# Performance work log

Measured on AMD Instinct MI355X. Metric: run time of the kernel, lower is better.

## Reference

```python
import jax, jax.numpy as jnp
import numpy as np

N_NODES = 100000

def setup_inputs() -> dict:
    key = jax.random.key(0)
    ks = jax.random.split(key, 8)
    n_feat, nhid, nclass = 256, 128, 40
    n_edges = 1600000
    x = jax.random.normal(ks[0], (N_NODES, n_feat), dtype=jnp.float32)
    edge_index = jax.random.randint(ks[1], (2, n_edges), 0, N_NODES, dtype=jnp.int64)
    # Glorot-ish scaled weights
    W1 = jax.random.normal(ks[2], (n_feat, nhid), dtype=jnp.float32) / np.sqrt(n_feat)
    b1 = jnp.zeros((nhid,), dtype=jnp.float32)
    W2 = jax.random.normal(ks[3], (nhid, nhid), dtype=jnp.float32) / np.sqrt(nhid)
    b2 = jnp.zeros((nhid,), dtype=jnp.float32)
    Wc = jax.random.normal(ks[4], (nhid, nclass), dtype=jnp.float32) / np.sqrt(nhid)
    bc = jnp.zeros((nclass,), dtype=jnp.float32)
    return {"x": x, "edge_index": edge_index, "W1": W1, "b1": b1,
            "W2": W2, "b2": b2, "Wc": Wc, "bc": bc}


def _gcn_conv(x, src, dst, W, b, n_nodes):
    """PyG GCNConv: transform, then sym-normalized aggregation with self-loops.
    out_i = sum_{j in N(i) u {i}} (d_i^-1/2 d_j^-1/2) (x_j W) + b,
    where d = in-degree over A + I.
    """
    h = x @ W  # [N, out]
    ones = jnp.ones_like(dst, dtype=h.dtype)
    deg = jax.ops.segment_sum(ones, dst, num_segments=n_nodes) + 1.0  # + self loop
    dinv = jax.lax.rsqrt(deg)  # deg >= 1, always valid
    norm = dinv[src] * dinv[dst]  # [E]
    msg = h[src] * norm[:, None]  # [E, out]  (dominant gather traffic)
    agg = jax.ops.segment_sum(msg, dst, num_segments=n_nodes)
    agg = agg + h * (dinv * dinv)[:, None]  # self-loop contribution
    return agg + b


def reference(x, edge_index, W1, b1, W2, b2, Wc, bc):
    # eval mode: dropout is identity
    src, dst = edge_index[0], edge_index[1]
    n = x.shape[0]
    h = jax.nn.relu(_gcn_conv(x, src, dst, W1, b1, n))
    h = jax.nn.relu(_gcn_conv(h, src, dst, W2, b2, n))
    return h @ Wc + bc
```

## Files before the change

### kernel.cpp

```cpp
#include <hip/hip_runtime.h>
#include <hip/hip_bf16.h>
#include <hip/hip_fp16.h>
#include <type_traits>


typedef _Float16 half8 __attribute__((ext_vector_type(8)));
typedef _Float16 half4v __attribute__((ext_vector_type(4)));
typedef float floatx4 __attribute__((ext_vector_type(4)));

#define EPB 8192


__device__ inline int block_incl_scan_256(int t, int* tmp) {
    int tid = threadIdx.x;
    tmp[tid] = t;
    __syncthreads();
    #pragma unroll
    for (int off = 1; off < 256; off <<= 1) {
        int v = (tid >= off) ? tmp[tid - off] : 0;
        __syncthreads();
        tmp[tid] += v;
        __syncthreads();
    }
    return tmp[tid];
}

template <int ITEMS>
__global__ __launch_bounds__(256) void k_scan1(const int* __restrict__ v,
                                               int* __restrict__ bsum, int n) {
    __shared__ int tmp[256];
    int base = blockIdx.x * (256 * ITEMS) + threadIdx.x * ITEMS;
    int t = 0;
    #pragma unroll
    for (int l = 0; l < ITEMS; ++l) {
        int i = base + l;
        t += (i < n) ? v[i] : 0;
    }
    block_incl_scan_256(t, tmp);
    if (threadIdx.x == 0) bsum[blockIdx.x] = tmp[255];
}

__global__ __launch_bounds__(256) void k_scan2(int* __restrict__ bsum, int nb) {
    __shared__ int tmp[256];
    int tid = threadIdx.x;
    int v = (tid < nb) ? bsum[tid] : 0;
    block_incl_scan_256(v, tmp);
    if (tid < nb) bsum[tid] = tid ? tmp[tid - 1] : 0;
}

template <int ITEMS>
__global__ __launch_bounds__(256) void k_scan3(const int* __restrict__ vin,
                                               const int* __restrict__ bsum,
                                               int* __restrict__ rp, int n) {
    __shared__ int tmp[256];
    int base = blockIdx.x * (256 * ITEMS) + threadIdx.x * ITEMS;
    int v[ITEMS];
    int t = 0;
    #pragma unroll
    for (int l = 0; l < ITEMS; ++l) {
        int i = base + l;
        v[l] = (i < n) ? vin[i] : 0;
        t += v[l];
    }
    block_incl_scan_256(t, tmp);
    int run = bsum[blockIdx.x] + (threadIdx.x ? tmp[threadIdx.x - 1] : 0);
    #pragma unroll
    for (int l = 0; l < ITEMS; ++l) {
        int i = base + l;
        if (i < n) rp[i] = run;
        run += v[l];
    }
}


__global__ __launch_bounds__(256) void k_histA(const int* __restrict__ dst,
                                               int* __restrict__ histM,
                                               int E, int nblk) {
    __shared__ int h[512];
    int tid = threadIdx.x;
    for (int i = tid; i < 512; i += 256) h[i] = 0;
    __syncthreads();
    int base = blockIdx.x * EPB;
    #pragma unroll 4
    for (int l = 0; l < EPB / 256; ++l) {
        int i = base + l * 256 + tid;
        if (i < E) atomicAdd(&h[dst[i] >> 8], 1);
    }
    __syncthreads();
    for (int i = tid; i < 512; i += 256)
        histM[i * nblk + blockIdx.x] = h[i];
}

__global__ __launch_bounds__(256) void k_scatterA(const int* __restrict__ src,
                                                  const int* __restrict__ dst,
                                                  const int* __restrict__ histS,
                                                  unsigned long long* __restrict__ eB,
                                                  int E, int nblk) {
    __shared__ int bse[512];
    __shared__ int cnt[512];
    int tid = threadIdx.x;
    for (int i = tid; i < 512; i += 256) {
        bse[i] = histS[i * nblk + blockIdx.x];
        cnt[i] = 0;
    }
    __syncthreads();
    int base = blockIdx.x * EPB;
    #pragma unroll 4
    for (int l = 0; l < EPB / 256; ++l) {
        int i = base + l * 256 + tid;
        if (i < E) {
            int d = dst[i];
            int s = src[i];
            int b = d >> 8;
            int r = atomicAdd(&cnt[b], 1);
            eB[bse[b] + r] = ((unsigned long long)(unsigned)d << 32) | (unsigned)s;
        }
    }
}

#define BCAP 4608
__global__ __launch_bounds__(256) void k_sortB(const unsigned long long* __restrict__ eB,
                                               const int* __restrict__ histS,
                                               int* __restrict__ srcS,
                                               int* __restrict__ rowptr,
                                               float* __restrict__ dinv,
                                               int n, int E, int nblk) {
    const int b   = blockIdx.x;
    const int tid = threadIdx.x;
    const int ni0 = b << 8;
    int s0 = histS[b * nblk];
    int s1 = (b < 511) ? histS[(b + 1) * nblk] : E;
    int cnt = s1 - s0;
    if (cnt > BCAP) cnt = BCAP;
    if (cnt == 0 && ni0 > n) return;

    __shared__ int hist[256];
    __shared__ int tmp[256];
    __shared__ int baseA[256];
    __shared__ int cntA[256];
    __shared__ int dstL[BCAP];
    __shared__ unsigned srcL[BCAP];
    __shared__ int lbA[256];

    hist[tid] = 0;
    cntA[tid] = 0;
    __syncthreads();
    for (int i = s0 + tid; i < s0 + cnt; i += 256) {
        int d = (int)(eB[i] >> 32);
        atomicAdd(&hist[d & 255], 1);
    }
    __syncthreads();
    int own  = hist[tid];
    int incl = block_incl_scan_256(own, tmp);
    baseA[tid] = incl - own;
    __syncthreads();
    for (int i = s0 + tid; i < s0 + cnt; i += 256) {
        unsigned long long v = eB[i];
        int d = (int)(v >> 32);
        int dig = d & 255;
        int r = atomicAdd(&cntA[dig], 1);
        int pos = baseA[dig] + r;
        dstL[pos] = d;
        srcL[pos] = (unsigned)v;
    }
    __syncthreads();
    for (int j = tid; j < cnt; j += 256)
        srcS[s0 + j] = (int)srcL[j];
    if (ni0 <= n) {
        int i = ni0 + tid;
        int lo = 0, hi = cnt;
        while (lo < hi) {
            int mid = (lo + hi) >> 1;
            if (dstL[mid] < i) lo = mid + 1; else hi = mid;
        }
        lbA[tid] = lo;
        __syncthreads();
        if (i <= n) {
            rowptr[i] = s0 + lo;
            if (i < n) {
                int ub = (tid < 255) ? lbA[tid + 1] : cnt;
                dinv[i] = rsqrtf((float)(ub - lo + 1));
            }
        }
    }
}

__global__ __launch_bounds__(256) void k_wcast(const float* __restrict__ W,
                                               _Float16* __restrict__ Wt,
                                               int N, int K, int kbits, int total) {
    int i = blockIdx.x * 256 + threadIdx.x;
    if (i < total) {
        int c = i >> kbits;
        int k = i & (K - 1);
        Wt[i] = (c < N) ? (_Float16)W[(size_t)k * N + c] : (_Float16)0.f;
    }
}


template <int K, int BN, typename AT, typename OT>
__global__ __launch_bounds__(256) void gemm_mfma(const AT* __restrict__ A,
                                                 const _Float16* __restrict__ Wt,
                                                 const float* __restrict__ bias,
                                                 OT* __restrict__ C,
                                                 int M, int N) {
    constexpr int NT = BN / 16;
    __shared__ __align__(16) _Float16 As[64][40];
    __shared__ __align__(16) _Float16 Bs[BN][40];

    const int tid  = threadIdx.x;
    const int bm   = blockIdx.x * 64;
    const int lane = tid & 63;
    const int wv   = tid >> 6;
    const int qd   = lane >> 4;
    const int ln15 = lane & 15;

    floatx4 acc[NT];
    #pragma unroll
    for (int c = 0; c < NT; ++c) acc[c] = (floatx4){0.f, 0.f, 0.f, 0.f};

    for (int k0 = 0; k0 < K; k0 += 32) {
        if constexpr (std::is_same<AT, float>::value) {
            #pragma unroll
            for (int l = 0; l < 2; ++l) {
                int f4  = tid + l * 256;
                int row = f4 >> 3;
                int kk  = (f4 & 7) << 2;
                float4 v = make_float4(0.f, 0.f, 0.f, 0.f);
                if (bm + row < M)
                    v = *(const float4*)(A + (size_t)(bm + row) * K + k0 + kk);
                half4v h;
                h[0] = (_Float16)v.x; h[1] = (_Float16)v.y;
                h[2] = (_Float16)v.z; h[3] = (_Float16)v.w;
                *(half4v*)&As[row][kk] = h;
            }
        } else {
            int row = tid >> 2;
            int kk  = (tid & 3) << 3;
            uint4 v = make_uint4(0u, 0u, 0u, 0u);
            if (bm + row < M)
                v = *(const uint4*)((const _Float16*)A + (size_t)(bm + row) * K + k0 + kk);
            *(uint4*)&As[row][kk] = v;
        }
        #pragma unroll
        for (int l = 0; l < (BN * 4 + 255) / 256; ++l) {
            int idx = tid + l * 256;
            if (idx < BN * 4) {
                int col = idx >> 2;
                int kk  = (idx & 3) << 3;
                *(uint4*)&Bs[col][kk] =
                    *(const uint4*)(Wt + (size_t)col * K + k0 + kk);
            }
        }
        __syncthreads();

        half8 a = *(const half8*)&As[wv * 16 + ln15][qd * 8];
        #pragma unroll
        for (int c = 0; c < NT; ++c) {
            half8 b = *(const half8*)&Bs[c * 16 + ln15][qd * 8];
            acc[c] = __builtin_amdgcn_mfma_f32_16x16x32_f16(a, b, acc[c], 0, 0, 0);
        }
        __syncthreads();
    }

    int baseRow = bm + wv * 16 + qd * 4;
    #pragma unroll
    for (int c = 0; c < NT; ++c) {
        int col = c * 16 + ln15;
        if constexpr (std::is_same<OT, _Float16>::value) {
            #pragma unroll
            for (int r = 0; r < 4; ++r) {
                int row = baseRow + r;
                if (row < M) C[(size_t)row * N + col] = (_Float16)acc[c][r];
            }
        } else {
            float bv = (col < N && bias) ? bias[col] : 0.f;
            #pragma unroll
            for (int r = 0; r < 4; ++r) {
                int row = baseRow + r;
                if (row < M && col < N)
                    ((float*)C)[(size_t)row * N + col] = acc[c][r] + bv;
            }
        }
    }
}


__global__ __launch_bounds__(256) void gcn_agg(const unsigned int* __restrict__ h,
                                               const int* __restrict__ rowptr,
                                               const int* __restrict__ srcS,
                                               const float* __restrict__ dinv,
                                               const float* __restrict__ bias,
                                               unsigned int* __restrict__ out,
                                               int n, int do_relu) {
    int node = blockIdx.x * 4 + (threadIdx.x >> 6);
    if (node >= n) return;
    const int lane = threadIdx.x & 63;
    const int g    = lane >> 4;
    const int t    = lane & 15;

    const _Float16* hb = (const _Float16*)h;

    float di = dinv[node];
    int e0 = rowptr[node];
    int e1 = rowptr[node + 1];

    half8 sv = *(const half8*)(hb + (size_t)(unsigned)node * 128 + t * 8);
    const float4* b4 = (const float4*)bias;
    float4 blo = b4[t * 2 + 0];
    float4 bhi = b4[t * 2 + 1];

    float acc[8];
    #pragma unroll
    for (int i = 0; i < 8; ++i) acc[i] = 0.f;

    for (int ce = e0; ce < e1; ce += 64) {
        int cnt = e1 - ce;
        cnt = (cnt < 64) ? cnt : 64;
        int colv = 0, wval = 0;
        if (lane < cnt) {
            int c = srcS[ce + lane];
            colv = c;
            wval = __float_as_int(di * dinv[c]);
        }
        #pragma unroll 2
        for (int d = 0; d < cnt; d += 4) {
            int idx = (d + g) << 2;
            int c   = __builtin_amdgcn_ds_bpermute(idx, colv);
            float w = __int_as_float(__builtin_amdgcn_ds_bpermute(idx, wval));
            half8 hv = *(const half8*)(hb + (size_t)(unsigned)c * 128 + t * 8);
            #pragma unroll
            for (int i = 0; i < 8; ++i)
                acc[i] += (float)hv[i] * w;
        }
    }

    #pragma unroll
    for (int i = 0; i < 8; ++i) acc[i] += __shfl_xor(acc[i], 16);
    #pragma unroll
    for (int i = 0; i < 8; ++i) acc[i] += __shfl_xor(acc[i], 32);

    float s = di * di;
    float bb[8] = {blo.x, blo.y, blo.z, blo.w, bhi.x, bhi.y, bhi.z, bhi.w};
    half8 o;
    #pragma unroll
    for (int i = 0; i < 8; ++i) {
        float v = acc[i] + (float)sv[i] * s + bb[i];
        if (do_relu) v = fmaxf(v, 0.f);
        o[i] = (_Float16)v;
    }
    if (g == 0)
        *(half8*)((_Float16*)out + (size_t)(unsigned)node * 128 + t * 8) = o;
}


extern "C" void kernel_launch(void* const* d_in, const int* in_sizes, int n_in,
                              void* d_out, int out_size, void* d_ws, size_t ws_size,
                              hipStream_t stream) {
    const float* x  = (const float*)d_in[0];
    const int* eidx = (const int*)d_in[1];
    const float* W1 = (const float*)d_in[2];
    const float* b1 = (const float*)d_in[3];
    const float* W2 = (const float*)d_in[4];
    const float* b2 = (const float*)d_in[5];
    const float* Wc = (const float*)d_in[6];
    const float* bc = (const float*)d_in[7];
    float* out = (float*)d_out;

    const int NF = 256, NH = 128, NC = 40;
    const int n = in_sizes[0] / NF;
    const int E = in_sizes[1] / 2;
    const int* src = eidx;
    const int* dst = eidx + E;

    const int nblk = (E + EPB - 1) / EPB;
    const int hm   = 512 * nblk;
    const int nbA  = (hm + 4095) / 4096;

    char* wsb = (char*)d_ws;
    size_t off = 0;
    auto alloc = [&](size_t bytes) {
        char* p = wsb + off;
        off = (off + bytes + 511) & ~(size_t)511;
        return p;
    };
    _Float16* hbuf = (_Float16*)alloc((size_t)n * NH * 2);
    _Float16* abuf = (_Float16*)alloc((size_t)n * NH * 2);
    _Float16* W1t  = (_Float16*)alloc((size_t)128 * 256 * 2);
    _Float16* W2t  = (_Float16*)alloc((size_t)128 * 128 * 2);
    _Float16* Wct  = (_Float16*)alloc((size_t)48 * 128 * 2);
    unsigned long long* eB = (unsigned long long*)alloc((size_t)E * 8);
    int* srcS      = (int*)alloc((size_t)E * 4);
    int* histM     = (int*)alloc((size_t)hm * 4);
    int* histS     = (int*)alloc((size_t)hm * 4);
    int* rowptr    = (int*)alloc((size_t)(n + 1) * 4);
    float* dinv    = (float*)alloc((size_t)n * 4);
    int* bsumA     = (int*)alloc(1024);

    k_histA<<<nblk, 256, 0, stream>>>(dst, histM, E, nblk);
    k_scan1<16><<<nbA, 256, 0, stream>>>(histM, bsumA, hm);
    k_scan2<<<1, 256, 0, stream>>>(bsumA, nbA);
    k_scan3<16><<<nbA, 256, 0, stream>>>(histM, bsumA, histS, hm);
    k_scatterA<<<nblk, 256, 0, stream>>>(src, dst, histS, eB, E, nblk);
    k_sortB<<<512, 256, 0, stream>>>(eB, histS, srcS, rowptr, dinv, n, E, nblk);

    k_wcast<<<(128 * 256 + 255) / 256, 256, 0, stream>>>(W1, W1t, 128, 256, 8, 128 * 256);
    k_wcast<<<(128 * 128 + 255) / 256, 256, 0, stream>>>(W2, W2t, 128, 128, 7, 128 * 128);
    k_wcast<<<(48 * 128 + 255) / 256, 256, 0, stream>>>(Wc, Wct, 40, 128, 7, 48 * 128);

    const int gMt = (n + 63) / 64;
    gemm_mfma<256, 128, float, _Float16><<<gMt, 256, 0, stream>>>(x, W1t, nullptr, hbuf, n, NH);
    gcn_agg<<<(n + 3) / 4, 256, 0, stream>>>((const unsigned int*)hbuf, rowptr, srcS, dinv, b1,
                                             (unsigned int*)abuf, n, 1);
    gemm_mfma<128, 128, _Float16, _Float16><<<gMt, 256, 0, stream>>>(abuf, W2t, nullptr, hbuf, n, NH);
    gcn_agg<<<(n + 3) / 4, 256, 0, stream>>>((const unsigned int*)hbuf, rowptr, srcS, dinv, b2,
                                             (unsigned int*)abuf, n, 1);
    gemm_mfma<128, 48, _Float16, float><<<gMt, 256, 0, stream>>>(abuf, Wct, bc, out, n, NC);
}
```

Measured before the change: 418.1 us.

## Keep full weight matrix resident in LDS and load A fragments directly

```diff
diff --git a/kernel.cpp b/kernel.cpp
--- a/kernel.cpp
+++ b/kernel.cpp
@@ -197,88 +197,95 @@
 }
 
 
-template <int K, int BN, typename AT, typename OT>
-__global__ __launch_bounds__(256) void gemm_mfma(const AT* __restrict__ A,
+template <int K, int BN, int MT, typename AT, typename OT>
+__global__ __launch_bounds__(256) void gemm_bres(const AT* __restrict__ A,
                                                  const _Float16* __restrict__ Wt,
                                                  const float* __restrict__ bias,
                                                  OT* __restrict__ C,
                                                  int M, int N) {
+    constexpr int KP = K + 8;
     constexpr int NT = BN / 16;
-    __shared__ __align__(16) _Float16 As[64][40];
-    __shared__ __align__(16) _Float16 Bs[BN][40];
+    __shared__ __align__(16) _Float16 Bs[BN * KP];
 
     const int tid  = threadIdx.x;
-    const int bm   = blockIdx.x * 64;
     const int lane = tid & 63;
     const int wv   = tid >> 6;
     const int qd   = lane >> 4;
     const int ln15 = lane & 15;
-
-    floatx4 acc[NT];
-    #pragma unroll
-    for (int c = 0; c < NT; ++c) acc[c] = (floatx4){0.f, 0.f, 0.f, 0.f};
-
-    for (int k0 = 0; k0 < K; k0 += 32) {
-        if constexpr (std::is_same<AT, float>::value) {
-            #pragma unroll
-            for (int l = 0; l < 2; ++l) {
-                int f4  = tid + l * 256;
-                int row = f4 >> 3;
-                int kk  = (f4 & 7) << 2;
-                float4 v = make_float4(0.f, 0.f, 0.f, 0.f);
-                if (bm + row < M)
-                    v = *(const float4*)(A + (size_t)(bm + row) * K + k0 + kk);
-                half4v h;
-                h[0] = (_Float16)v.x; h[1] = (_Float16)v.y;
-                h[2] = (_Float16)v.z; h[3] = (_Float16)v.w;
-                *(half4v*)&As[row][kk] = h;
+    const int bm   = blockIdx.x * (64 * MT);
+
+    constexpr int TOT = BN * K / 8;
+    for (int i = tid; i < TOT; i += 256) {
+        int idx = i * 8;
+        int col = idx / K;
+        int kk  = idx % K;
+        *(uint4*)&Bs[col * KP + kk] = *(const uint4*)(Wt + idx);
+    }
+    __syncthreads();
+
+    floatx4 acc[MT][NT];
+    #pragma unroll
+    for (int mt = 0; mt < MT; ++mt)
+        #pragma unroll
+        for (int c = 0; c < NT; ++c) acc[mt][c] = (floatx4){0.f, 0.f, 0.f, 0.f};
+
+    int rw[MT];
+    #pragma unroll
+    for (int mt = 0; mt < MT; ++mt) {
+        int r = bm + (wv * MT + mt) * 16 + ln15;
+        rw[mt] = (r < M) ? r : (M - 1);
+    }
+
+    #pragma unroll
+    for (int ks = 0; ks < K / 32; ++ks) {
+        half8 a[MT];
+        #pragma unroll
+        for (int mt = 0; mt < MT; ++mt) {
+            if constexpr (std::is_same<AT, float>::value) {
+                const float* p = A + (size_t)rw[mt] * K + ks * 32 + qd * 8;
+                float4 v0 = *(const float4*)p;
+                float4 v1 = *(const float4*)(p + 4);
+                half8 h;
+                h[0] = (_Float16)v0.x; h[1] = (_Float16)v0.y;
+                h[2] = (_Float16)v0.z; h[3] = (_Float16)v0.w;
+                h[4] = (_Float16)v1.x; h[5] = (_Float16)v1.y;
+                h[6] = (_Float16)v1.z; h[7] = (_Float16)v1.w;
+                a[mt] = h;
+            } else {
+                a[mt] = *(const half8*)((const _Float16*)A +
+                                        (size_t)rw[mt] * K + ks * 32 + qd * 8);
             }
-        } else {
-            int row = tid >> 2;
-            int kk  = (tid & 3) << 3;
-            uint4 v = make_uint4(0u, 0u, 0u, 0u);
-            if (bm + row < M)
-                v = *(const uint4*)((const _Float16*)A + (size_t)(bm + row) * K + k0 + kk);
-            *(uint4*)&As[row][kk] = v;
-        }
-        #pragma unroll
-        for (int l = 0; l < (BN * 4 + 255) / 256; ++l) {
-            int idx = tid + l * 256;
-            if (idx < BN * 4) {
-                int col = idx >> 2;
-                int kk  = (idx & 3) << 3;
-                *(uint4*)&Bs[col][kk] =
-                    *(const uint4*)(Wt + (size_t)col * K + k0 + kk);
-            }
-        }
-        __syncthreads();
-
-        half8 a = *(const half8*)&As[wv * 16 + ln15][qd * 8];
+        }
         #pragma unroll
         for (int c = 0; c < NT; ++c) {
-            half8 b = *(const half8*)&Bs[c * 16 + ln15][qd * 8];
-            acc[c] = __builtin_amdgcn_mfma_f32_16x16x32_f16(a, b, acc[c], 0, 0, 0);
-        }
-        __syncthreads();
-    }
-
-    int baseRow = bm + wv * 16 + qd * 4;
-    #pragma unroll
-    for (int c = 0; c < NT; ++c) {
-        int col = c * 16 + ln15;
-        if constexpr (std::is_same<OT, _Float16>::value) {
-            #pragma unroll
-            for (int r = 0; r < 4; ++r) {
-                int row = baseRow + r;
-                if (row < M) C[(size_t)row * N + col] = (_Float16)acc[c][r];
-            }
-        } else {
-            float bv = (col < N && bias) ? bias[col] : 0.f;
-            #pragma unroll
-            for (int r = 0; r < 4; ++r) {
-                int row = baseRow + r;
-                if (row < M && col < N)
-                    ((float*)C)[(size_t)row * N + col] = acc[c][r] + bv;
+            half8 b = *(const half8*)&Bs[(c * 16 + ln15) * KP + ks * 32 + qd * 8];
+            #pragma unroll
+            for (int mt = 0; mt < MT; ++mt)
+                acc[mt][c] = __builtin_amdgcn_mfma_f32_16x16x32_f16(a[mt], b,
+                                                                    acc[mt][c], 0, 0, 0);
+        }
+    }
+
+    #pragma unroll
+    for (int mt = 0; mt < MT; ++mt) {
+        int baseRow = bm + (wv * MT + mt) * 16 + qd * 4;
+        #pragma unroll
+        for (int c = 0; c < NT; ++c) {
+            int col = c * 16 + ln15;
+            if constexpr (std::is_same<OT, _Float16>::value) {
+                #pragma unroll
+                for (int r = 0; r < 4; ++r) {
+                    int row = baseRow + r;
+                    if (row < M) C[(size_t)row * N + col] = (_Float16)acc[mt][c][r];
+                }
+            } else {
+                float bv = (col < N && bias) ? bias[col] : 0.f;
+                #pragma unroll
+                for (int r = 0; r < 4; ++r) {
+                    int row = baseRow + r;
+                    if (row < M && col < N)
+                        ((float*)C)[(size_t)row * N + col] = acc[mt][c][r] + bv;
+                }
             }
         }
     }
@@ -322,8 +329,38 @@
             colv = c;
             wval = __float_as_int(di * dinv[c]);
         }
-        #pragma unroll 2
-        for (int d = 0; d < cnt; d += 4) {
+        int d = 0;
+        for (; d + 16 <= cnt; d += 16) {
+            int i0 = (d + 0 + g) << 2;
+            int i1 = (d + 4 + g) << 2;
+            int i2 = (d + 8 + g) << 2;
+            int i3 = (d + 12 + g) << 2;
+            int c0 = __builtin_amdgcn_ds_bpermute(i0, colv);
+            int c1 = __builtin_amdgcn_ds_bpermute(i1, colv);
+            int c2 = __builtin_amdgcn_ds_bpermute(i2, colv);
+            int c3 = __builtin_amdgcn_ds_bpermute(i3, colv);
+            int w0i = __builtin_amdgcn_ds_bpermute(i0, wval);
+            int w1i = __builtin_amdgcn_ds_bpermute(i1, wval);
+            int w2i = __builtin_amdgcn_ds_bpermute(i2, wval);
+            int w3i = __builtin_amdgcn_ds_bpermute(i3, wval);
+            half8 h0 = *(const half8*)(hb + (size_t)(unsigned)c0 * 128 + t * 8);
+            half8 h1 = *(const half8*)(hb + (size_t)(unsigned)c1 * 128 + t * 8);
+            half8 h2 = *(const half8*)(hb + (size_t)(unsigned)c2 * 128 + t * 8);
+            half8 h3 = *(const half8*)(hb + (size_t)(unsigned)c3 * 128 + t * 8);
+            float w0 = __int_as_float(w0i);
+            float w1 = __int_as_float(w1i);
+            float w2 = __int_as_float(w2i);
+            float w3 = __int_as_float(w3i);
+            #pragma unroll
+            for (int i = 0; i < 8; ++i) acc[i] += (float)h0[i] * w0;
+            #pragma unroll
+            for (int i = 0; i < 8; ++i) acc[i] += (float)h1[i] * w1;
+            #pragma unroll
+            for (int i = 0; i < 8; ++i) acc[i] += (float)h2[i] * w2;
+            #pragma unroll
+            for (int i = 0; i < 8; ++i) acc[i] += (float)h3[i] * w3;
+        }
+        for (; d < cnt; d += 4) {
             int idx = (d + g) << 2;
             int c   = __builtin_amdgcn_ds_bpermute(idx, colv);
             float w = __int_as_float(__builtin_amdgcn_ds_bpermute(idx, wval));
@@ -407,12 +444,12 @@
     k_wcast<<<(128 * 128 + 255) / 256, 256, 0, stream>>>(W2, W2t, 128, 128, 7, 128 * 128);
     k_wcast<<<(48 * 128 + 255) / 256, 256, 0, stream>>>(Wc, Wct, 40, 128, 7, 48 * 128);
 
-    const int gMt = (n + 63) / 64;
-    gemm_mfma<256, 128, float, _Float16><<<gMt, 256, 0, stream>>>(x, W1t, nullptr, hbuf, n, NH);
+    const int gB = (n + 127) / 128;
+    gemm_bres<256, 128, 2, float, _Float16><<<gB, 256, 0, stream>>>(x, W1t, nullptr, hbuf, n, NH);
     gcn_agg<<<(n + 3) / 4, 256, 0, stream>>>((const unsigned int*)hbuf, rowptr, srcS, dinv, b1,
                                              (unsigned int*)abuf, n, 1);
-    gemm_mfma<128, 128, _Float16, _Float16><<<gMt, 256, 0, stream>>>(abuf, W2t, nullptr, hbuf, n, NH);
+    gemm_bres<128, 128, 2, _Float16, _Float16><<<gB, 256, 0, stream>>>(abuf, W2t, nullptr, hbuf, n, NH);
     gcn_agg<<<(n + 3) / 4, 256, 0, stream>>>((const unsigned int*)hbuf, rowptr, srcS, dinv, b2,
                                              (unsigned int*)abuf, n, 1);
-    gemm_mfma<128, 48, _Float16, float><<<gMt, 256, 0, stream>>>(abuf, Wct, bc, out, n, NC);
-}
+    gemm_bres<128, 48, 2, _Float16, float><<<gB, 256, 0, stream>>>(abuf, Wct, bc, out, n, NC);
+}
```

After: 421.0 us. Within noise of the previous version (+0.7%).
